# Optimization experiments

Measured on AMD Instinct MI355X. Metric: run time of the kernel, lower is better.

Reference implementation:

```python
import jax, jax.numpy as jnp
import numpy as np

FIELD_DIMS = (339, 5825, 64)
RANK = 128
NUM_CHANNELS = 256
BATCH = 131072
NUM_MODES = len(FIELD_DIMS)


def setup_inputs() -> dict:
    key = jax.random.key(0)
    ks = jax.random.split(key, 12)
    # per-mode in-range indices, shape (B, num_modes)
    cols = [jax.random.randint(ks[i], (BATCH,), 0, FIELD_DIMS[i]) for i in range(NUM_MODES)]
    indices = jnp.stack(cols, axis=1).astype(jnp.int64)
    # embedding tables (one per tensor mode)
    emb0 = jax.random.normal(ks[3], (FIELD_DIMS[0], RANK), jnp.float32) * 0.1
    emb1 = jax.random.normal(ks[4], (FIELD_DIMS[1], RANK), jnp.float32) * 0.1
    emb2 = jax.random.normal(ks[5], (FIELD_DIMS[2], RANK), jnp.float32) * 0.1
    # conv1: Conv2d(1, C, kernel=(rank,1)) -> weight (C, rank) after squeeze
    w1 = jax.random.normal(ks[6], (NUM_CHANNELS, RANK), jnp.float32) * (1.0 / np.sqrt(RANK))
    b1 = jnp.zeros((NUM_CHANNELS,), jnp.float32)
    # conv2: Conv2d(C, C, kernel=(1,num_modes)) -> weight (C_out, C_in, num_modes)
    w2 = jax.random.normal(ks[7], (NUM_CHANNELS, NUM_CHANNELS, NUM_MODES), jnp.float32) * (1.0 / np.sqrt(NUM_CHANNELS * NUM_MODES))
    b2 = jnp.zeros((NUM_CHANNELS,), jnp.float32)
    # aggregation MLP
    wfc1 = jax.random.normal(ks[8], (NUM_CHANNELS, NUM_CHANNELS), jnp.float32) * (1.0 / np.sqrt(NUM_CHANNELS))
    bfc1 = jnp.zeros((NUM_CHANNELS,), jnp.float32)
    wfc2 = jax.random.normal(ks[9], (1, NUM_CHANNELS), jnp.float32) * (1.0 / np.sqrt(NUM_CHANNELS))
    bfc2 = jnp.zeros((1,), jnp.float32)
    return {"indices": indices, "emb0": emb0, "emb1": emb1, "emb2": emb2,
            "w1": w1, "b1": b1, "w2": w2, "b2": b2,
            "wfc1": wfc1, "bfc1": bfc1, "wfc2": wfc2, "bfc2": bfc2}


def reference(indices, emb0, emb1, emb2, w1, b1, w2, b2, wfc1, bfc1, wfc2, bfc2):
    # EmbeddingModule: (B, rank, num_modes)
    x = jnp.stack([emb0[indices[:, 0]], emb1[indices[:, 1]], emb2[indices[:, 2]]], axis=2)
    # conv1 over rank dim (kernel (rank,1)): (B, C, num_modes)
    h = jax.nn.relu(jnp.einsum('brm,cr->bcm', x, w1) + b1[None, :, None])
    # conv2 over mode dim (kernel (1,num_modes)): (B, C)
    h = jax.nn.relu(jnp.einsum('bcm,dcm->bd', h, w2) + b2)
    # AggregationModule MLP
    h = jax.nn.relu(h @ wfc1.T + bfc1)
    out = jax.nn.relu(h @ wfc2.T + bfc2)  # (B, 1)
    return out.squeeze(-1)  # (B,)
```

## Files before the change

### kernel.cpp

```cpp
#include <hip/hip_runtime.h>

typedef __bf16 bf16;
typedef __bf16 bf16x4 __attribute__((ext_vector_type(4)));
typedef __bf16 bf16x8 __attribute__((ext_vector_type(8)));
typedef float  f32x4  __attribute__((ext_vector_type(4)));
typedef unsigned int uint32;

#define BT 64

#define N_EF0 (22*2048)
#define N_EF1 (365*2048)
#define N_EF2 (4*2048)
#define O_EF0 0
#define O_EF1 (O_EF0+N_EF0)
#define O_EF2 (O_EF1+N_EF1)
#define O_W1F (O_EF2+N_EF2)
#define O_W2F (O_W1F+32768)
#define O_F1  (O_W2F+196608)
#define O_F2  (O_F1+65536)
#define N_TOT (O_F2+256)

#define BYTES_BF16 ((size_t)N_TOT*2)
#define OFF_FLOAT  BYTES_BF16
#define OFF_FLAG   (OFF_FLOAT + 772*4)
#define OFF_IDX    (OFF_FLAG + 16)
#define N_IDX      (131072*3)
#define OFF_Q      (OFF_IDX + (size_t)N_IDX*4)

#define QB0 0
#define QB1 (339*256)
#define QB2 (QB1 + 5825*256)

static __device__ __forceinline__ f32x4 mfma16(bf16x8 a, bf16x8 b, f32x4 c) {
    return __builtin_amdgcn_mfma_f32_16x16x32_bf16(a, b, c, 0, 0, 0);
}

static __device__ __forceinline__ unsigned frag_off(unsigned ee, unsigned kk, unsigned nks) {
    return (((ee >> 4) * nks + (kk >> 5)) * 64u + ((kk >> 3) & 3u) * 16u + (ee & 15u)) * 8u
           + (kk & 7u);
}

__global__ __launch_bounds__(256)
void convert_all(const void* __restrict__ e0, const void* __restrict__ e1,
                 const void* __restrict__ e2, const void* __restrict__ w1r,
                 const void* __restrict__ b1r, const void* __restrict__ w2r,
                 const void* __restrict__ b2r, const void* __restrict__ f1r,
                 const void* __restrict__ fc1br, const void* __restrict__ f2r,
                 const void* __restrict__ fc2br, const void* __restrict__ idxr,
                 bf16* __restrict__ wsb, float* __restrict__ wsf,
                 int* __restrict__ flagp, int* __restrict__ idx32)
{
    __shared__ int sF;
    const int tid = threadIdx.x;
    const int bid = blockIdx.x;
    if (tid == 0) sF = 0;
    __syncthreads();

    if (bid < 256) {
        if (((const uint32*)idxr)[tid * 2 + 1] != 0) atomicOr(&sF, 1);
        __syncthreads();
        const bool i64 = (sF == 0);
        #pragma unroll
        for (int it = 0; it < 6; ++it) {
            int k = bid * 1536 + it * 256 + tid;
            if (k < N_IDX) {
                long long v = i64 ? ((const long long*)idxr)[k]
                                  : (long long)((const int*)idxr)[k];
                int m = k - (k / 3) * 3;
                long long dim = (m == 0 ? 339 : (m == 1 ? 5825 : 64));
                v = v < 0 ? 0 : (v >= dim ? dim - 1 : v);
                idx32[k] = (int)v;
            }
        }
        return;
    }

    if (tid < 64) {
        uint32 e = (((const uint32*)w1r)[tid] >> 7) & 0xffu;
        if (e > 126u) atomicOr(&sF, 1);
    }
    __syncthreads();
    const bool fp32 = (sF != 0);

    if (bid < 768) {
        const unsigned n4 = 895744u / 4u;
        for (unsigned u = (bid - 256) * 256u + tid; u < n4; u += 512u * 256u) {
            unsigned e = u * 4;
            const void* src; unsigned off, dst;
            if (e < 829952u) {
                unsigned base;
                if (e < 43392u)       { src = e0;  off = e;           base = O_EF0; }
                else if (e < 788992u) { src = e1;  off = e - 43392u;  base = O_EF1; }
                else if (e < 797184u) { src = e2;  off = e - 788992u; base = O_EF2; }
                else                  { src = w1r; off = e - 797184u; base = O_W1F; }
                dst = base + frag_off(off >> 7, off & 127u, 4u);
            } else if (e < 895488u) {
                src = f1r; off = e - 829952u;
                dst = O_F1 + frag_off(off >> 8, off & 255u, 8u);
            } else {
                src = f2r; off = e - 895488u; dst = O_F2 + off;
            }
            if (fp32) {
                float4 v = *(const float4*)((const float*)src + off);
                bf16x4 o; o[0]=(bf16)v.x; o[1]=(bf16)v.y; o[2]=(bf16)v.z; o[3]=(bf16)v.w;
                *(bf16x4*)(wsb + dst) = o;
            } else {
                *(uint2*)(wsb + dst) = *(const uint2*)((const bf16*)src + off);
            }
        }
    } else if (bid < 1008) {
        for (unsigned i = (bid - 768) * 256u + tid; i < 196608u; i += 240u * 256u) {
            unsigned m = i >> 16, r = i & 65535u;
            unsigned dt = r >> 12, ks = (r >> 9) & 7u, lane = (r >> 3) & 63u, j = r & 7u;
            unsigned d = dt * 16u + (lane & 15u);
            unsigned c = ks * 32u + (lane >> 4) * 8u + j;
            unsigned off = d * 768u + c * 3u + m;
            wsb[O_W2F + i] = fp32 ? (bf16)((const float*)w2r)[off] : ((const bf16*)w2r)[off];
        }
    } else {
        if (tid == 0) *flagp = fp32 ? 1 : 0;
        #pragma unroll
        for (int it = 0; it < 4; ++it) {
            int j = it * 256 + tid;
            if (j < 769) {
                const void* src; int off;
                if (j < 256)      { src = b1r;   off = j; }
                else if (j < 512) { src = b2r;   off = j - 256; }
                else if (j < 768) { src = fc1br; off = j - 512; }
                else              { src = fc2br; off = 0; }
                wsf[j] = fp32 ? ((const float*)src)[off] : (float)((const bf16*)src)[off];
            }
        }
    }
}

__global__ __launch_bounds__(256)
void build_q(const bf16* __restrict__ wsb, const float* __restrict__ wsf,
             bf16* __restrict__ Qt)
{
    __shared__ alignas(16) bf16 sPE[4096];

    const int tid  = threadIdx.x;
    const int wave = tid >> 6;
    const int lane = tid & 63;
    const int quad = lane >> 4;
    const int l15  = lane & 15;
    const int bid  = blockIdx.x;

    int m, tile, dim, efBase, qBase;
    if (bid < 22)       { m = 0; tile = bid;       dim = 339;  efBase = O_EF0; qBase = QB0; }
    else if (bid < 387) { m = 1; tile = bid - 22;  dim = 5825; efBase = O_EF1; qBase = QB1; }
    else                { m = 2; tile = bid - 387; dim = 64;   efBase = O_EF2; qBase = QB2; }
    const int row0 = tile * 16;

    const bf16* w1f = wsb + O_W1F;
    const bf16* w2f = wsb + O_W2F + m * 65536;
    const float* fb1 = wsf;
    const f32x4 zero4 = {0.f, 0.f, 0.f, 0.f};

    bf16x8 be[4];
    #pragma unroll
    for (int ks = 0; ks < 4; ++ks)
        be[ks] = *(const bf16x8*)(wsb + efBase + (size_t)((tile * 4 + ks) * 64 + lane) * 8);

    #pragma unroll
    for (int mtl = 0; mtl < 4; ++mtl) {
        int mt = wave * 4 + mtl;
        f32x4 acc = zero4;
        #pragma unroll
        for (int ks = 0; ks < 4; ++ks) {
            bf16x8 aw = *(const bf16x8*)(w1f + ((mt * 4 + ks) * 64 + lane) * 8);
            acc = mfma16(aw, be[ks], acc);
        }
        const float4 bv = *(const float4*)(fb1 + mt * 16 + quad * 4);
        bf16x4 hv;
        hv[0] = (bf16)fmaxf(acc[0] + bv.x, 0.f);
        hv[1] = (bf16)fmaxf(acc[1] + bv.y, 0.f);
        hv[2] = (bf16)fmaxf(acc[2] + bv.z, 0.f);
        hv[3] = (bf16)fmaxf(acc[3] + bv.w, 0.f);
        int ksq   = mt >> 1;
        int quadq = ((mt & 1) << 1) | (quad >> 1);
        int j0    = (quad & 1) * 4;
        *(bf16x4*)(&sPE[(ksq * 64 + quadq * 16 + l15) * 8 + j0]) = hv;
    }
    __syncthreads();

    f32x4 acc2[4];
    #pragma unroll
    for (int nt = 0; nt < 4; ++nt) acc2[nt] = zero4;
    #pragma unroll
    for (int ks = 0; ks < 8; ++ks) {
        bf16x8 af = *(const bf16x8*)(&sPE[(ks * 64 + lane) * 8]);
        #pragma unroll
        for (int nt = 0; nt < 4; ++nt) {
            bf16x8 bw = *(const bf16x8*)(w2f + (size_t)(((wave * 4 + nt) * 8 + ks) * 64 + lane) * 8);
            acc2[nt] = mfma16(af, bw, acc2[nt]);
        }
    }
    #pragma unroll
    for (int nt = 0; nt < 4; ++nt) {
        int d = (wave * 4 + nt) * 16 + l15;
        #pragma unroll
        for (int r = 0; r < 4; ++r) {
            int rl = quad * 4 + r;
            if (row0 + rl < dim)
                Qt[qBase + (size_t)(row0 + rl) * 256 + d] = (bf16)acc2[nt][r];
        }
    }
}

__global__ __launch_bounds__(256, 4)
void costco_main(const bf16* __restrict__ wsb, const bf16* __restrict__ Qt,
                 const float* __restrict__ wsf, const int* __restrict__ flagp,
                 const int* __restrict__ idx32, void* __restrict__ out)
{
    __shared__ alignas(16) bf16 sH2[BT * 264];
    __shared__ float sPart[4][BT];
    __shared__ int sIdx[BT * 3];

    const bf16* wf   = wsb + O_F1;
    const bf16* wfc2 = wsb + O_F2;
    const float* fb2  = wsf + 256;
    const float* fbc1 = wsf + 512;
    const float  bfc2v = wsf[768];
    const int fp32out = *flagp;

    const int tid  = threadIdx.x;
    const int wave = tid >> 6;
    const int lane = tid & 63;
    const int quad = lane >> 4;
    const int l15  = lane & 15;
    const int bbase = blockIdx.x * BT;

    if (tid < BT * 3) sIdx[tid] = idx32[bbase * 3 + tid];
    __syncthreads();

    {
        const int half = lane >> 5;
        const int l31  = lane & 31;
        float bb[8];
        {
            float4 t0 = *(const float4*)(fb2 + l31 * 8);
            float4 t1 = *(const float4*)(fb2 + l31 * 8 + 4);
            bb[0]=t0.x; bb[1]=t0.y; bb[2]=t0.z; bb[3]=t0.w;
            bb[4]=t1.x; bb[5]=t1.y; bb[6]=t1.z; bb[7]=t1.w;
        }
        #pragma unroll
        for (int rp = 0; rp < 8; ++rp) {
            const int r  = wave * 16 + rp * 2 + half;
            const int i0 = sIdx[r * 3 + 0];
            const int i1 = sIdx[r * 3 + 1];
            const int i2 = sIdx[r * 3 + 2];
            bf16x8 a = *(const bf16x8*)(Qt + QB0 + (size_t)i0 * 256 + l31 * 8);
            bf16x8 b = *(const bf16x8*)(Qt + QB1 + (size_t)i1 * 256 + l31 * 8);
            bf16x8 c = *(const bf16x8*)(Qt + QB2 + (size_t)i2 * 256 + l31 * 8);
            bf16x8 o;
            #pragma unroll
            for (int j = 0; j < 8; ++j) {
                float v = (float)a[j] + (float)b[j] + (float)c[j] + bb[j];
                o[j] = (bf16)fmaxf(v, 0.f);
            }
            *(bf16x8*)(&sH2[r * 264 + l31 * 8]) = o;
        }
    }
    __syncthreads();

    const f32x4 zero4 = {0.f, 0.f, 0.f, 0.f};

    f32x4 acc3[4][4];
    #pragma unroll
    for (int i = 0; i < 4; ++i)
        #pragma unroll
        for (int j = 0; j < 4; ++j) acc3[i][j] = zero4;
    #pragma unroll
    for (int ks = 0; ks < 8; ++ks) {
        bf16x8 af[4], bfr[4];
        #pragma unroll
        for (int mt = 0; mt < 4; ++mt)
            af[mt] = *(const bf16x8*)(&sH2[(mt * 16 + l15) * 264 + ks * 32 + quad * 8]);
        #pragma unroll
        for (int nt = 0; nt < 4; ++nt)
            bfr[nt] = *(const bf16x8*)(wf + ((size_t)((wave * 4 + nt) * 8 + ks) * 64 + lane) * 8);
        #pragma unroll
        for (int mt = 0; mt < 4; ++mt)
            #pragma unroll
            for (int nt = 0; nt < 4; ++nt)
                acc3[mt][nt] = mfma16(af[mt], bfr[nt], acc3[mt][nt]);
    }

    float wv[4], bc[4];
    #pragma unroll
    for (int nt = 0; nt < 4; ++nt) {
        int e = wave * 64 + nt * 16 + l15;
        wv[nt] = (float)wfc2[e];
        bc[nt] = fbc1[e];
    }
    #pragma unroll
    for (int mt = 0; mt < 4; ++mt)
        #pragma unroll
        for (int r = 0; r < 4; ++r) {
            float p = 0.f;
            #pragma unroll
            for (int nt = 0; nt < 4; ++nt)
                p += fmaxf(acc3[mt][nt][r] + bc[nt], 0.f) * wv[nt];
            p += __shfl_xor(p, 1, 64);
            p += __shfl_xor(p, 2, 64);
            p += __shfl_xor(p, 4, 64);
            p += __shfl_xor(p, 8, 64);
            if (l15 == 0) sPart[wave][mt * 16 + quad * 4 + r] = p;
        }
    __syncthreads();

    if (tid < BT) {
        float v = sPart[0][tid] + sPart[1][tid] + sPart[2][tid] + sPart[3][tid] + bfc2v;
        v = fmaxf(v, 0.f);
        if (fp32out) ((float*)out)[bbase + tid] = v;
        else         ((bf16*)out)[bbase + tid] = (bf16)v;
    }
}

extern "C" void kernel_launch(void* const* d_in, const int* in_sizes, int n_in,
                              void* d_out, int out_size, void* d_ws, size_t ws_size,
                              hipStream_t stream) {
    char* ws = (char*)d_ws;
    bf16*  wsb   = (bf16*)ws;
    float* wsf   = (float*)(ws + OFF_FLOAT);
    int*   flagp = (int*)(ws + OFF_FLAG);
    int*   idx32 = (int*)(ws + OFF_IDX);
    bf16*  Qt    = (bf16*)(ws + OFF_Q);

    hipLaunchKernelGGL(convert_all, dim3(1009), dim3(256), 0, stream,
                       d_in[1], d_in[2], d_in[3], d_in[4], d_in[5], d_in[6],
                       d_in[7], d_in[8], d_in[9], d_in[10], d_in[11], d_in[0],
                       wsb, wsf, flagp, idx32);

    hipLaunchKernelGGL(build_q, dim3(391), dim3(256), 0, stream, wsb, wsf, Qt);

    const int B = 131072;
    hipLaunchKernelGGL(costco_main, dim3(B / BT), dim3(256), 0, stream,
                       wsb, Qt, wsf, flagp, idx32, d_out);
}
```

Before: 117.8 us.

## Fold conv2 bias into Q table, swizzle sH2 layout, drop index staging

Folds the conv2 bias into the mode-0 precomputed Q table, which removes the per-element bias add in the gather stage. Indices are now loaded directly from global memory into registers instead of being staged through shared memory, which removes one block barrier. The gathered activations are stored in an XOR-swizzled, fragment-ordered shared layout so the MFMA operand reads map to contiguous 16-byte chunks without padding. The first FC1 weight fragment is prefetched before the barrier so its latency overlaps the sync. The cost is more index registers per thread and more involved shared-memory address arithmetic.

```diff
diff --git a/kernel.cpp b/kernel.cpp
--- a/kernel.cpp
+++ b/kernel.cpp
@@ -156,6 +156,7 @@
     const bf16* w1f = wsb + O_W1F;
     const bf16* w2f = wsb + O_W2F + m * 65536;
     const float* fb1 = wsf;
+    const float* fb2 = wsf + 256;
     const f32x4 zero4 = {0.f, 0.f, 0.f, 0.f};
 
     bf16x8 be[4];
@@ -200,11 +201,12 @@
     #pragma unroll
     for (int nt = 0; nt < 4; ++nt) {
         int d = (wave * 4 + nt) * 16 + l15;
+        const float addb = (m == 0) ? fb2[d] : 0.f;
         #pragma unroll
         for (int r = 0; r < 4; ++r) {
             int rl = quad * 4 + r;
             if (row0 + rl < dim)
-                Qt[qBase + (size_t)(row0 + rl) * 256 + d] = (bf16)acc2[nt][r];
+                Qt[qBase + (size_t)(row0 + rl) * 256 + d] = (bf16)(acc2[nt][r] + addb);
         }
     }
 }
@@ -214,13 +216,11 @@
                  const float* __restrict__ wsf, const int* __restrict__ flagp,
                  const int* __restrict__ idx32, void* __restrict__ out)
 {
-    __shared__ alignas(16) bf16 sH2[BT * 264];
+    __shared__ alignas(16) bf16 sH2[BT * 256];
     __shared__ float sPart[4][BT];
-    __shared__ int sIdx[BT * 3];
 
     const bf16* wf   = wsb + O_F1;
     const bf16* wfc2 = wsb + O_F2;
-    const float* fb2  = wsf + 256;
     const float* fbc1 = wsf + 512;
     const float  bfc2v = wsf[768];
     const int fp32out = *flagp;
@@ -232,37 +232,38 @@
     const int l15  = lane & 15;
     const int bbase = blockIdx.x * BT;
 
-    if (tid < BT * 3) sIdx[tid] = idx32[bbase * 3 + tid];
-    __syncthreads();
-
     {
-        const int half = lane >> 5;
-        const int l31  = lane & 31;
-        float bb[8];
-        {
-            float4 t0 = *(const float4*)(fb2 + l31 * 8);
-            float4 t1 = *(const float4*)(fb2 + l31 * 8 + 4);
-            bb[0]=t0.x; bb[1]=t0.y; bb[2]=t0.z; bb[3]=t0.w;
-            bb[4]=t1.x; bb[5]=t1.y; bb[6]=t1.z; bb[7]=t1.w;
-        }
+        const int half  = lane >> 5;
+        const int l31   = lane & 31;
+        const int ksw   = l31 >> 2;
+        const int quadw = l31 & 3;
+        int i0[8], i1[8], i2[8];
         #pragma unroll
         for (int rp = 0; rp < 8; ++rp) {
-            const int r  = wave * 16 + rp * 2 + half;
-            const int i0 = sIdx[r * 3 + 0];
-            const int i1 = sIdx[r * 3 + 1];
-            const int i2 = sIdx[r * 3 + 2];
-            bf16x8 a = *(const bf16x8*)(Qt + QB0 + (size_t)i0 * 256 + l31 * 8);
-            bf16x8 b = *(const bf16x8*)(Qt + QB1 + (size_t)i1 * 256 + l31 * 8);
-            bf16x8 c = *(const bf16x8*)(Qt + QB2 + (size_t)i2 * 256 + l31 * 8);
+            const int gb = (bbase + wave * 16 + rp * 2 + half) * 3;
+            i0[rp] = idx32[gb];
+            i1[rp] = idx32[gb + 1];
+            i2[rp] = idx32[gb + 2];
+        }
+        #pragma unroll
+        for (int rp = 0; rp < 8; ++rp) {
+            bf16x8 a = *(const bf16x8*)(Qt + QB0 + (size_t)i0[rp] * 256 + l31 * 8);
+            bf16x8 b = *(const bf16x8*)(Qt + QB1 + (size_t)i1[rp] * 256 + l31 * 8);
+            bf16x8 c = *(const bf16x8*)(Qt + QB2 + (size_t)i2[rp] * 256 + l31 * 8);
             bf16x8 o;
             #pragma unroll
-            for (int j = 0; j < 8; ++j) {
-                float v = (float)a[j] + (float)b[j] + (float)c[j] + bb[j];
-                o[j] = (bf16)fmaxf(v, 0.f);
-            }
-            *(bf16x8*)(&sH2[r * 264 + l31 * 8]) = o;
-        }
-    }
+            for (int j = 0; j < 8; ++j)
+                o[j] = (bf16)fmaxf((float)a[j] + (float)b[j] + (float)c[j], 0.f);
+            const int l15r = rp * 2 + half;
+            *(bf16x8*)(&sH2[((wave * 8 + ksw) * 64 + quadw * 16 + (l15r ^ ksw)) * 8]) = o;
+        }
+    }
+
+    bf16x8 bfr0[4];
+    #pragma unroll
+    for (int nt = 0; nt < 4; ++nt)
+        bfr0[nt] = *(const bf16x8*)(wf + ((size_t)((wave * 4 + nt) * 8) * 64 + lane) * 8);
+
     __syncthreads();
 
     const f32x4 zero4 = {0.f, 0.f, 0.f, 0.f};
@@ -277,10 +278,11 @@
         bf16x8 af[4], bfr[4];
         #pragma unroll
         for (int mt = 0; mt < 4; ++mt)
-            af[mt] = *(const bf16x8*)(&sH2[(mt * 16 + l15) * 264 + ks * 32 + quad * 8]);
+            af[mt] = *(const bf16x8*)(&sH2[((mt * 8 + ks) * 64 + quad * 16 + (l15 ^ ks)) * 8]);
         #pragma unroll
         for (int nt = 0; nt < 4; ++nt)
-            bfr[nt] = *(const bf16x8*)(wf + ((size_t)((wave * 4 + nt) * 8 + ks) * 64 + lane) * 8);
+            bfr[nt] = (ks == 0) ? bfr0[nt]
+                    : *(const bf16x8*)(wf + ((size_t)((wave * 4 + nt) * 8 + ks) * 64 + lane) * 8);
         #pragma unroll
         for (int mt = 0; mt < 4; ++mt)
             #pragma unroll
```

After: 117.6 us, median of 2. About the same (-0.2%).
